# Kernel tuning notes

Measured on AMD Instinct MI355X. Metric: run time of the kernel, lower is better.

## Reference

```python
import jax, jax.numpy as jnp
import numpy as np

B, DIM, H, W = 4, 192, 256, 256
HEADS, DS = 6, 2
CPH = DIM // HEADS  # channels per head = 32
DN = ('NCHW', 'OIHW', 'NCHW')


def _conv(x, w, padding, groups=1):
    return jax.lax.conv_general_dilated(x, w, (1, 1), padding,
                                        dimension_numbers=DN,
                                        feature_group_count=groups)


def setup_inputs() -> dict:
    key = jax.random.key(0)
    ks = jax.random.split(key, 5)
    x = jax.random.normal(ks[0], (B, DIM, H, W), dtype=jnp.float32)
    temperature = jnp.ones((HEADS, 1, 1), dtype=jnp.float32)
    qkv_w = jax.random.normal(ks[1], (3 * DIM, DIM, 1, 1), dtype=jnp.float32) * 0.02
    dw_w = jax.random.normal(ks[2], (3 * DIM, 1, 3, 3), dtype=jnp.float32) * 0.02
    proj_w = jax.random.normal(ks[3], (DIM, DIM, 1, 1), dtype=jnp.float32) * 0.02
    a = jnp.full((1,), 0.2, dtype=jnp.float32)
    return {"x": x, "temperature": temperature, "qkv_w": qkv_w, "dw_w": dw_w,
            "proj_w": proj_w, "a1": a, "a2": a, "a3": a, "a4": a}


def _masked_softmax(attn, kk):
    # top-k mask per row (exact torch.topk + scatter_ semantics)
    _, idx = jax.lax.top_k(attn, kk)                      # [b,h,C,kk]
    mask = jax.nn.one_hot(idx, attn.shape[-1], dtype=jnp.bool_).any(axis=-2)
    return jax.nn.softmax(jnp.where(mask, attn, -jnp.inf), axis=-1)


def reference(x, temperature, qkv_w, dw_w, proj_w, a1, a2, a3, a4):
    b, c, h, w = x.shape
    h2, w2 = h // DS, w // DS
    # 1x1 qkv conv at full res, then exact adaptive (regular) max pool by DS
    qkv = _conv(x, qkv_w, 'VALID')                        # [b, 3*dim, h, w]
    qkv = jax.lax.reduce_window(qkv, -jnp.inf, jax.lax.max,
                                (1, 1, DS, DS), (1, 1, DS, DS), 'VALID')
    # depthwise 3x3
    qkv = _conv(qkv, dw_w, 'SAME', groups=3 * DIM)        # [b, 3*dim, h2, w2]
    q, k, v = jnp.split(qkv, 3, axis=1)
    n = h2 * w2
    q = q.reshape(b, HEADS, CPH, n)
    k = k.reshape(b, HEADS, CPH, n)
    v = v.reshape(b, HEADS, CPH, n)
    # F.normalize along last dim (eps clamp 1e-12)
    q = q / jnp.maximum(jnp.linalg.norm(q, axis=-1, keepdims=True), 1e-12)
    k = k / jnp.maximum(jnp.linalg.norm(k, axis=-1, keepdims=True), 1e-12)
    attn = jnp.einsum('bhcn,bhdn->bhcd', q, k) * temperature[None]  # [b,h,C,C]
    Cc = attn.shape[-1]
    att1 = _masked_softmax(attn, Cc // 2)
    att2 = _masked_softmax(attn, Cc * 2 // 3)
    att3 = _masked_softmax(attn, Cc * 3 // 4)
    att4 = _masked_softmax(attn, Cc * 4 // 5)
    def apply(a):
        return jnp.einsum('bhcd,bhdn->bhcn', a, v)
    out = apply(att1) * a1 + apply(att2) * a2 + apply(att3) * a3 + apply(att4) * a4
    out = out.reshape(b, DIM, h2, w2)
    out = jax.nn.gelu(out, approximate=False)
    # nearest upsample by integer factor DS
    out = jnp.repeat(jnp.repeat(out, DS, axis=2), DS, axis=3)
    out = _conv(out, proj_w, 'VALID')
    return out
```

## Files before the change

kernel.cpp:

```cpp
#include <hip/hip_runtime.h>
#include <hip/hip_bf16.h>
#include <math.h>

typedef __attribute__((ext_vector_type(8))) short bf16x8;
typedef __attribute__((ext_vector_type(4))) float f32x4;
typedef __attribute__((ext_vector_type(4))) unsigned int u32x4;

#define NP 16384
#define HWFULL 65536

__device__ __forceinline__ unsigned short f2bf(float f){
    union { float f; unsigned int u; } v; v.f = f;
    unsigned int u = v.u;
    u += 0x7fffu + ((u >> 16) & 1u);
    return (unsigned short)(u >> 16);
}
__device__ __forceinline__ float bf2f(unsigned short h){
    union { unsigned int u; float f; } v; v.u = ((unsigned int)h) << 16;
    return v.f;
}
__device__ __forceinline__ unsigned int pk2(float a, float b){
    return (unsigned int)f2bf(a) | ((unsigned int)f2bf(b) << 16);
}

__global__ void k_convert(const float* __restrict__ s, unsigned short* __restrict__ d, int n){
    int i = blockIdx.x * 256 + threadIdx.x;
    if (i < n) d[i] = f2bf(s[i]);
}

__global__ __launch_bounds__(256, 2)
void k_qkvpool(const float* __restrict__ x, const unsigned short* __restrict__ Wbf,
               unsigned short* __restrict__ qkvp){
    __shared__ unsigned short Bl[128*200];
    __shared__ unsigned short Ep[192*36];
    int tid = threadIdx.x;
    int lane = tid & 63, wv = tid >> 6;
    int n16 = lane & 15, quad = lane >> 4;
    int bx = blockIdx.x;
    int y2 = bx >> 2, x2blk = bx & 3;
    int b = blockIdx.y;

    #pragma unroll 6
    for (int j=0;j<12;j++){
        int idx = tid + j*256;
        int g = idx >> 7, w = idx & 127;
        int y = y2*2 + (w >> 6);
        int xc = x2blk*64 + (w & 63);
        const float* xp = x + (size_t)(b*192 + g*8) * HWFULL + y*256 + xc;
        float v0 = xp[0];
        float v1 = xp[(size_t)1*HWFULL];
        float v2 = xp[(size_t)2*HWFULL];
        float v3 = xp[(size_t)3*HWFULL];
        float v4 = xp[(size_t)4*HWFULL];
        float v5 = xp[(size_t)5*HWFULL];
        float v6 = xp[(size_t)6*HWFULL];
        float v7 = xp[(size_t)7*HWFULL];
        u32x4 pk;
        pk.x = pk2(v0,v1); pk.y = pk2(v2,v3); pk.z = pk2(v4,v5); pk.w = pk2(v6,v7);
        *(u32x4*)&Bl[w*200 + g*8] = pk;
    }
    bf16x8 afc[3], afn[3];
    #pragma unroll
    for (int j=0;j<3;j++)
        afc[j] = *(const bf16x8*)(Wbf + (size_t)(((wv*3+j)*16 + n16)*192 + quad*8));
    __syncthreads();

    for (int ocblk=0; ocblk<3; ocblk++){
        f32x4 acc[3][8];
        #pragma unroll
        for (int j=0;j<3;j++)
          #pragma unroll
          for (int s=0;s<8;s++)
            acc[j][s] = (f32x4){0.f,0.f,0.f,0.f};

        #pragma unroll 1
        for (int it=0; it<6; it++){
            int nocb = (it==5) ? ocblk+1 : ocblk;
            int nit  = (it==5) ? 0 : it+1;
            if (nocb < 3){
                #pragma unroll
                for (int j=0;j<3;j++)
                    afn[j] = *(const bf16x8*)(Wbf +
                        (size_t)((nocb*192 + (wv*3+j)*16 + n16)*192 + nit*32 + quad*8));
            }
            int bko = it*32 + quad*8;
            bf16x8 bfr[8];
            #pragma unroll
            for (int s=0;s<8;s++) bfr[s] = *(const bf16x8*)&Bl[(s*16 + n16)*200 + bko];
            #pragma unroll
            for (int j=0;j<3;j++)
              #pragma unroll
              for (int s=0;s<8;s++)
                acc[j][s] = __builtin_amdgcn_mfma_f32_16x16x32_bf16(afc[j], bfr[s], acc[j][s], 0,0,0);
            #pragma unroll
            for (int j=0;j<3;j++) afc[j] = afn[j];
        }
        __syncthreads();
        #pragma unroll
        for (int j=0;j<3;j++){
            int ocr = (wv*3+j)*16 + quad*4;
            #pragma unroll
            for (int sp=0;sp<4;sp++){
                #pragma unroll
                for (int r=0;r<4;r++){
                    float v = fmaxf(acc[j][sp][r], acc[j][sp+4][r]);
                    float o = __shfl_xor(v, 1, 64);
                    v = fmaxf(v, o);
                    if ((n16 & 1) == 0)
                        Ep[(ocr + r)*36 + sp*8 + (n16 >> 1)] = f2bf(v);
                }
            }
        }
        __syncthreads();
        size_t rowbase = (size_t)(b*576 + ocblk*192)*NP + y2*128 + x2blk*32;
        #pragma unroll
        for (int it=0; it<6; it++){
            int c = tid + it*256;
            int row = c >> 3, seg = c & 7;
            uint2 vv = *(const uint2*)&Ep[row*36 + seg*4];
            *(uint2*)(qkvp + rowbase + (size_t)row*NP + seg*4) = vv;
        }
    }
}

__global__ void k_dwconv(const unsigned short* __restrict__ qkvp, const float* __restrict__ dww,
                         float* __restrict__ dwout, float* __restrict__ sumsq){
    __shared__ float sl[18*130];
    int tid = threadIdx.x;
    int y0 = blockIdx.x * 16;
    int ch = blockIdx.y;
    int b  = blockIdx.z;
    const unsigned short* in = qkvp + (size_t)(b*576 + ch) * NP;
    #pragma unroll
    for (int j=0;j<10;j++){
        int idx = tid + j*256;
        if (idx < 18*130){
            int row = idx / 130;
            int col = idx % 130;
            int gy = y0 - 1 + row;
            int gx = col - 1;
            float v = 0.f;
            if (gy >= 0 && gy < 128 && gx >= 0 && gx < 128)
                v = bf2f(in[gy*128 + gx]);
            sl[idx] = v;
        }
    }
    float w0 = dww[ch*9+0], w1 = dww[ch*9+1], w2 = dww[ch*9+2];
    float w3 = dww[ch*9+3], w4 = dww[ch*9+4], w5 = dww[ch*9+5];
    float w6 = dww[ch*9+6], w7 = dww[ch*9+7], w8 = dww[ch*9+8];
    __syncthreads();
    float* outp = dwout + (size_t)(b*576 + ch) * NP;
    int col = tid & 127, half = tid >> 7;
    float ssq = 0.f;
    #pragma unroll
    for (int i=0;i<8;i++){
        int ry = half*8 + i;
        const float* r0 = &sl[ry*130 + col];
        float a = r0[0]*w0   + r0[1]*w1   + r0[2]*w2
                + r0[130]*w3 + r0[131]*w4 + r0[132]*w5
                + r0[260]*w6 + r0[261]*w7 + r0[262]*w8;
        outp[(y0+ry)*128 + col] = a;
        ssq += a*a;
    }
    if (ch < 384){
        #pragma unroll
        for (int off=32; off>0; off>>=1) ssq += __shfl_down(ssq, off, 64);
        if ((tid & 63) == 0) atomicAdd(&sumsq[b*384 + ch], ssq);
    }
}

__global__ __launch_bounds__(256) void k_attnraw(const float* __restrict__ dwout,
                                                 float* __restrict__ attn){
    __shared__ float sq[128*34];
    __shared__ float sk[128*34];
    int tid = threadIdx.x;
    int n0 = blockIdx.x * 512;
    int h = blockIdx.y, b = blockIdx.z;
    const float* qb = dwout + (size_t)(b*576 + h*32)*NP + n0;
    const float* kb = dwout + (size_t)(b*576 + 192 + h*32)*NP + n0;
    int s = tid >> 6, l = tid & 63;
    int c0 = (l & 7) * 4, d0 = (l >> 3) * 4;
    float acc[4][4];
    #pragma unroll
    for (int i=0;i<4;i++)
      #pragma unroll
      for (int j=0;j<4;j++) acc[i][j] = 0.f;

    for (int slc=0; slc<4; slc++){
        int nb = slc*128;
        __syncthreads();
        #pragma unroll 4
        for (int j=0;j<16;j++){
            int idx = tid + j*256;
            int r = idx >> 7, c = idx & 127;
            sq[c*34 + r] = qb[(size_t)r*NP + nb + c];
            sk[c*34 + r] = kb[(size_t)r*NP + nb + c];
        }
        __syncthreads();
        #pragma unroll 4
        for (int i=0;i<32;i++){
            int n = s*32 + i;
            const float* qp = &sq[n*34];
            const float* kp = &sk[n*34];
            float2 qa = *(const float2*)(qp + c0);
            float2 qc = *(const float2*)(qp + c0 + 2);
            float2 ka = *(const float2*)(kp + d0);
            float2 kc = *(const float2*)(kp + d0 + 2);
            float qv[4] = {qa.x, qa.y, qc.x, qc.y};
            float kv[4] = {ka.x, ka.y, kc.x, kc.y};
            #pragma unroll
            for (int ci=0;ci<4;ci++)
              #pragma unroll
              for (int di=0;di<4;di++)
                acc[ci][di] += qv[ci]*kv[di];
        }
    }
    __syncthreads();
    float* red = sq;
    #pragma unroll
    for (int ci=0;ci<4;ci++)
      #pragma unroll
      for (int di=0;di<4;di++)
        red[(s*32 + c0+ci)*33 + d0+di] = acc[ci][di];
    __syncthreads();
    float* ap = attn + (size_t)(b*6+h)*1024;
    #pragma unroll
    for (int j=0;j<4;j++){
        int o = tid + j*256;
        int c = o >> 5, d = o & 31;
        float v = red[(0*32 + c)*33 + d] + red[(1*32 + c)*33 + d]
                + red[(2*32 + c)*33 + d] + red[(3*32 + c)*33 + d];
        atomicAdd(ap + o, v);
    }
}

__global__ void k_mask_softmax(const float* __restrict__ attn, const float* __restrict__ sumsq,
                               const float* __restrict__ temp,
                               const float* __restrict__ A1, const float* __restrict__ A2,
                               const float* __restrict__ A3, const float* __restrict__ A4,
                               float* __restrict__ comb){
    __shared__ float Am[32][33];
    __shared__ float Em[32][33];
    __shared__ float qn[32], kn[32];
    __shared__ unsigned char Rm[32][32];
    int t = threadIdx.x;
    int bh = blockIdx.x;
    int b = bh / 6, h = bh % 6;
    if (t < 32){
        qn[t] = fmaxf(sqrtf(sumsq[b*384 + h*32 + t]), 1e-12f);
        kn[t] = fmaxf(sqrtf(sumsq[b*384 + 192 + h*32 + t]), 1e-12f);
    }
    __syncthreads();
    float tv = temp[h];
    const float* ap = attn + (size_t)bh*1024;
    #pragma unroll
    for (int j=0;j<16;j++){
        int idx = t + j*64;
        int c = idx >> 5, d = idx & 31;
        Am[c][d] = ap[idx] * tv / (qn[c]*kn[d]);
    }
    __syncthreads();
    if (t < 32){
        int c = t;
        float m = -1e30f;
        for (int d=0;d<32;d++) m = fmaxf(m, Am[c][d]);
        for (int d=0;d<32;d++) Em[c][d] = expf(Am[c][d] - m);
        for (int d=0;d<32;d++){
            float ad = Am[c][d];
            int rk = 0;
            for (int dd=0;dd<32;dd++){
                float av = Am[c][dd];
                rk += (av > ad) || (av == ad && dd < d);
            }
            Rm[c][d] = (unsigned char)rk;
        }
        float d0=0,d1=0,d2=0,d3=0;
        for (int d=0;d<32;d++){
            float e = Em[c][d]; int rk = Rm[c][d];
            if (rk < 16) d0 += e;
            if (rk < 21) d1 += e;
            if (rk < 24) d2 += e;
            if (rk < 25) d3 += e;
        }
        float f0 = A1[0]/d0, f1 = A2[0]/d1, f2 = A3[0]/d2, f3 = A4[0]/d3;
        float* cp = comb + (size_t)bh*1024 + c*32;
        for (int d=0;d<32;d++){
            int rk = Rm[c][d];
            float s = (rk<16?f0:0.f) + (rk<21?f1:0.f) + (rk<24?f2:0.f) + (rk<25?f3:0.f);
            cp[d] = Em[c][d] * s;
        }
    }
}

__global__ void k_applyv(const float* __restrict__ dwout, const float* __restrict__ comb,
                         unsigned short* __restrict__ gT){
    __shared__ float cm[3072];
    int tid = threadIdx.x;
    int b = blockIdx.y;
    int hz = blockIdx.z * 3;
    int n = blockIdx.x*256 + tid;
    #pragma unroll
    for (int j=0;j<12;j++) cm[tid + j*256] = comb[b*6144 + hz*1024 + tid + j*256];
    __syncthreads();
    const float* vb = dwout + (size_t)(b*576 + 384 + hz*32)*NP + n;
    unsigned short* gp = gT + (size_t)(b*NP + n)*192 + hz*32;
    #pragma unroll 1
    for (int h=0;h<3;h++){
        float v[32];
        #pragma unroll
        for (int d=0;d<32;d++) v[d] = vb[(size_t)(h*32+d)*NP];
        const float* chp = &cm[h*1024];
        #pragma unroll 1
        for (int cg=0;cg<4;cg++){
            float s[8];
            #pragma unroll
            for (int i=0;i<8;i++){
                const float* crow = chp + (cg*8+i)*32;
                float acc = 0.f;
                #pragma unroll
                for (int d=0;d<32;d++) acc += crow[d]*v[d];
                s[i] = 0.5f*acc*(1.f + erff(acc*0.70710678118654752f));
            }
            u32x4 pk;
            pk.x = pk2(s[0],s[1]); pk.y = pk2(s[2],s[3]);
            pk.z = pk2(s[4],s[5]); pk.w = pk2(s[6],s[7]);
            *(u32x4*)(gp + h*32 + cg*8) = pk;
        }
    }
}

__global__ __launch_bounds__(256, 2)
void k_proj(const unsigned short* __restrict__ gT, const unsigned short* __restrict__ Pbf,
            float* __restrict__ out){
    __shared__ unsigned short Bl[128*200];
    int tid = threadIdx.x;
    int lane = tid & 63, wv = tid >> 6;
    int n16 = lane & 15, quad = lane >> 4;
    int y2 = blockIdx.x, b = blockIdx.y;

    #pragma unroll 6
    for (int j=0;j<12;j++){
        int idx = tid + j*256;
        int r = idx / 24, g = idx - r*24;
        *(u32x4*)&Bl[r*200 + g*8] =
            *(const u32x4*)(gT + ((size_t)(b*NP + y2*128 + r)*192 + g*8));
    }
    bf16x8 afc[3], afn[3];
    #pragma unroll
    for (int j=0;j<3;j++)
        afc[j] = *(const bf16x8*)(Pbf + (size_t)(((wv*3+j)*16 + n16)*192 + quad*8));
    __syncthreads();

    f32x4 acc[3][8];
    #pragma unroll
    for (int j=0;j<3;j++)
      #pragma unroll
      for (int s=0;s<8;s++)
        acc[j][s] = (f32x4){0.f,0.f,0.f,0.f};

    #pragma unroll 1
    for (int it=0; it<6; it++){
        if (it < 5){
            #pragma unroll
            for (int j=0;j<3;j++)
                afn[j] = *(const bf16x8*)(Pbf +
                    (size_t)(((wv*3+j)*16 + n16)*192 + (it+1)*32 + quad*8));
        }
        int bko = it*32 + quad*8;
        bf16x8 bfr[8];
        #pragma unroll
        for (int s=0;s<8;s++) bfr[s] = *(const bf16x8*)&Bl[(s*16 + n16)*200 + bko];
        #pragma unroll
        for (int j=0;j<3;j++)
          #pragma unroll
          for (int s=0;s<8;s++)
            acc[j][s] = __builtin_amdgcn_mfma_f32_16x16x32_bf16(afc[j], bfr[s], acc[j][s], 0,0,0);
        #pragma unroll
        for (int j=0;j<3;j++) afc[j] = afn[j];
    }

    #pragma unroll
    for (int j=0;j<3;j++){
        int oc = (wv*3+j)*16 + quad*4;
        #pragma unroll
        for (int sp=0;sp<8;sp++){
            int x2 = sp*16 + n16;
            #pragma unroll
            for (int r=0;r<4;r++){
                float v = acc[j][sp][r];
                size_t o = ((size_t)(b*192 + oc + r)*256 + 2*y2)*256 + 2*x2;
                float2 val = make_float2(v, v);
                *(float2*)(out + o) = val;
                *(float2*)(out + o + 256) = val;
            }
        }
    }
}

extern "C" void kernel_launch(void* const* d_in, const int* in_sizes, int n_in,
                              void* d_out, int out_size, void* d_ws, size_t ws_size,
                              hipStream_t stream){
    const float* x     = (const float*)d_in[0];
    const float* temp  = (const float*)d_in[1];
    const float* qkvw  = (const float*)d_in[2];
    const float* dww   = (const float*)d_in[3];
    const float* projw = (const float*)d_in[4];
    const float* A1    = (const float*)d_in[5];
    const float* A2    = (const float*)d_in[6];
    const float* A3    = (const float*)d_in[7];
    const float* A4    = (const float*)d_in[8];
    float* out = (float*)d_out;
    char* ws = (char*)d_ws;

    float*          dwout = (float*)ws;
    unsigned short* qkvp  = (unsigned short*)(ws + 150994944ull);
    unsigned short* gT    = (unsigned short*)(ws + 150994944ull);
    unsigned short* Wbf   = (unsigned short*)(ws + 226492416ull);
    unsigned short* Pbf   = (unsigned short*)(ws + 226713600ull);
    float*          attn  = (float*)(ws + 226787328ull);
    float*          comb  = (float*)(ws + 226885632ull);
    float*          sumsq = (float*)(ws + 226983936ull);

    hipMemsetAsync(attn, 0, 98304, stream);
    hipMemsetAsync(sumsq, 0, 6144, stream);
    k_convert<<<dim3((110592+255)/256), dim3(256), 0, stream>>>(qkvw, Wbf, 110592);
    k_convert<<<dim3((36864+255)/256), dim3(256), 0, stream>>>(projw, Pbf, 36864);
    k_qkvpool<<<dim3(512,4), dim3(256), 0, stream>>>(x, Wbf, qkvp);
    k_dwconv<<<dim3(8,576,4), dim3(256), 0, stream>>>(qkvp, dww, dwout, sumsq);
    k_attnraw<<<dim3(32,6,4), dim3(256), 0, stream>>>(dwout, attn);
    k_mask_softmax<<<dim3(24), dim3(64), 0, stream>>>(attn, sumsq, temp, A1, A2, A3, A4, comb);
    k_applyv<<<dim3(64,4,2), dim3(256), 0, stream>>>(dwout, comb, gT);
    k_proj<<<dim3(128,4), dim3(256), 0, stream>>>(gT, Pbf, out);
}
```

Measured before the change: 643.9 us.

## Store depthwise output in bf16, parallelize masked softmax, vectorize dwconv loads

```diff
diff --git a/kernel.cpp b/kernel.cpp
--- a/kernel.cpp
+++ b/kernel.cpp
@@ -20,7 +20,9 @@
     return v.f;
 }
 __device__ __forceinline__ unsigned int pk2(float a, float b){
-    return (unsigned int)f2bf(a) | ((unsigned int)f2bf(b) << 16);
+    unsigned int r;
+    asm("v_cvt_pk_bf16_f32 %0, %1, %2" : "=v"(r) : "v"(a), "v"(b));
+    return r;
 }
 
 __global__ void k_convert(const float* __restrict__ s, unsigned short* __restrict__ d, int n){
@@ -114,8 +116,8 @@
         __syncthreads();
         size_t rowbase = (size_t)(b*576 + ocblk*192)*NP + y2*128 + x2blk*32;
         #pragma unroll
-        for (int it=0; it<6; it++){
-            int c = tid + it*256;
+        for (int it2=0; it2<6; it2++){
+            int c = tid + it2*256;
             int row = c >> 3, seg = c & 7;
             uint2 vv = *(const uint2*)&Ep[row*36 + seg*4];
             *(uint2*)(qkvp + rowbase + (size_t)row*NP + seg*4) = vv;
@@ -124,43 +126,51 @@
 }
 
 __global__ void k_dwconv(const unsigned short* __restrict__ qkvp, const float* __restrict__ dww,
-                         float* __restrict__ dwout, float* __restrict__ sumsq){
-    __shared__ float sl[18*130];
+                         unsigned short* __restrict__ dwoutB, float* __restrict__ sumsq){
+    __shared__ float sl[18*132];
     int tid = threadIdx.x;
     int y0 = blockIdx.x * 16;
     int ch = blockIdx.y;
     int b  = blockIdx.z;
     const unsigned short* in = qkvp + (size_t)(b*576 + ch) * NP;
-    #pragma unroll
-    for (int j=0;j<10;j++){
-        int idx = tid + j*256;
-        if (idx < 18*130){
-            int row = idx / 130;
-            int col = idx % 130;
+    int l = tid & 63, wr = tid >> 6;
+    #pragma unroll
+    for (int j=0;j<5;j++){
+        int row = wr + j*4;
+        if (row < 18){
             int gy = y0 - 1 + row;
-            int gx = col - 1;
-            float v = 0.f;
-            if (gy >= 0 && gy < 128 && gx >= 0 && gx < 128)
-                v = bf2f(in[gy*128 + gx]);
-            sl[idx] = v;
-        }
-    }
+            float2 v = make_float2(0.f, 0.f);
+            if (gy >= 0 && gy < 128){
+                unsigned int u = *(const unsigned int*)&in[gy*128 + l*2];
+                v.x = bf2f((unsigned short)(u & 0xffffu));
+                v.y = bf2f((unsigned short)(u >> 16));
+            }
+            *(float2*)&sl[row*132 + 2 + l*2] = v;
+        }
+    }
+    if (tid < 18) sl[tid*132 + 1] = 0.f;
+    else if (tid < 36) sl[(tid-18)*132 + 130] = 0.f;
     float w0 = dww[ch*9+0], w1 = dww[ch*9+1], w2 = dww[ch*9+2];
     float w3 = dww[ch*9+3], w4 = dww[ch*9+4], w5 = dww[ch*9+5];
     float w6 = dww[ch*9+6], w7 = dww[ch*9+7], w8 = dww[ch*9+8];
     __syncthreads();
-    float* outp = dwout + (size_t)(b*576 + ch) * NP;
+    unsigned short* outp = dwoutB + (size_t)(b*576 + ch) * NP;
     int col = tid & 127, half = tid >> 7;
     float ssq = 0.f;
+    int base = (half*8)*132 + col + 1;
+    float r0a=sl[base],     r0b=sl[base+1],   r0c=sl[base+2];
+    float r1a=sl[base+132], r1b=sl[base+133], r1c=sl[base+134];
     #pragma unroll
     for (int i=0;i<8;i++){
-        int ry = half*8 + i;
-        const float* r0 = &sl[ry*130 + col];
-        float a = r0[0]*w0   + r0[1]*w1   + r0[2]*w2
-                + r0[130]*w3 + r0[131]*w4 + r0[132]*w5
-                + r0[260]*w6 + r0[261]*w7 + r0[262]*w8;
-        outp[(y0+ry)*128 + col] = a;
+        const float* r2 = &sl[base + (i+2)*132];
+        float r2a=r2[0], r2b=r2[1], r2c=r2[2];
+        float a = r0a*w0 + r0b*w1 + r0c*w2
+                + r1a*w3 + r1b*w4 + r1c*w5
+                + r2a*w6 + r2b*w7 + r2c*w8;
+        outp[(y0 + half*8 + i)*128 + col] = f2bf(a);
         ssq += a*a;
+        r0a=r1a; r0b=r1b; r0c=r1c;
+        r1a=r2a; r1b=r2b; r1c=r2c;
     }
     if (ch < 384){
         #pragma unroll
@@ -169,15 +179,15 @@
     }
 }
 
-__global__ __launch_bounds__(256) void k_attnraw(const float* __restrict__ dwout,
+__global__ __launch_bounds__(256) void k_attnraw(const unsigned short* __restrict__ dwoutB,
                                                  float* __restrict__ attn){
     __shared__ float sq[128*34];
     __shared__ float sk[128*34];
     int tid = threadIdx.x;
     int n0 = blockIdx.x * 512;
     int h = blockIdx.y, b = blockIdx.z;
-    const float* qb = dwout + (size_t)(b*576 + h*32)*NP + n0;
-    const float* kb = dwout + (size_t)(b*576 + 192 + h*32)*NP + n0;
+    const unsigned short* qb = dwoutB + (size_t)(b*576 + h*32)*NP + n0;
+    const unsigned short* kb = dwoutB + (size_t)(b*576 + 192 + h*32)*NP + n0;
     int s = tid >> 6, l = tid & 63;
     int c0 = (l & 7) * 4, d0 = (l >> 3) * 4;
     float acc[4][4];
@@ -193,8 +203,8 @@
         for (int j=0;j<16;j++){
             int idx = tid + j*256;
             int r = idx >> 7, c = idx & 127;
-            sq[c*34 + r] = qb[(size_t)r*NP + nb + c];
-            sk[c*34 + r] = kb[(size_t)r*NP + nb + c];
+            sq[c*34 + r] = bf2f(qb[(size_t)r*NP + nb + c]);
+            sk[c*34 + r] = bf2f(kb[(size_t)r*NP + nb + c]);
         }
         __syncthreads();
         #pragma unroll 4
@@ -240,59 +250,48 @@
                                const float* __restrict__ A3, const float* __restrict__ A4,
                                float* __restrict__ comb){
     __shared__ float Am[32][33];
-    __shared__ float Em[32][33];
     __shared__ float qn[32], kn[32];
-    __shared__ unsigned char Rm[32][32];
     int t = threadIdx.x;
     int bh = blockIdx.x;
     int b = bh / 6, h = bh % 6;
-    if (t < 32){
-        qn[t] = fmaxf(sqrtf(sumsq[b*384 + h*32 + t]), 1e-12f);
-        kn[t] = fmaxf(sqrtf(sumsq[b*384 + 192 + h*32 + t]), 1e-12f);
-    }
-    __syncthreads();
+    if (t < 32) qn[t] = fmaxf(sqrtf(sumsq[b*384 + h*32 + t]), 1e-12f);
+    else if (t >= 64 && t < 96) kn[t-64] = fmaxf(sqrtf(sumsq[b*384 + 192 + h*32 + (t-64)]), 1e-12f);
+    __syncthreads();
+    int c = t >> 5, d = t & 31;
     float tv = temp[h];
-    const float* ap = attn + (size_t)bh*1024;
-    #pragma unroll
-    for (int j=0;j<16;j++){
-        int idx = t + j*64;
-        int c = idx >> 5, d = idx & 31;
-        Am[c][d] = ap[idx] * tv / (qn[c]*kn[d]);
-    }
-    __syncthreads();
-    if (t < 32){
-        int c = t;
-        float m = -1e30f;
-        for (int d=0;d<32;d++) m = fmaxf(m, Am[c][d]);
-        for (int d=0;d<32;d++) Em[c][d] = expf(Am[c][d] - m);
-        for (int d=0;d<32;d++){
-            float ad = Am[c][d];
-            int rk = 0;
-            for (int dd=0;dd<32;dd++){
-                float av = Am[c][dd];
-                rk += (av > ad) || (av == ad && dd < d);
-            }
-            Rm[c][d] = (unsigned char)rk;
-        }
-        float d0=0,d1=0,d2=0,d3=0;
-        for (int d=0;d<32;d++){
-            float e = Em[c][d]; int rk = Rm[c][d];
-            if (rk < 16) d0 += e;
-            if (rk < 21) d1 += e;
-            if (rk < 24) d2 += e;
-            if (rk < 25) d3 += e;
-        }
-        float f0 = A1[0]/d0, f1 = A2[0]/d1, f2 = A3[0]/d2, f3 = A4[0]/d3;
-        float* cp = comb + (size_t)bh*1024 + c*32;
-        for (int d=0;d<32;d++){
-            int rk = Rm[c][d];
-            float s = (rk<16?f0:0.f) + (rk<21?f1:0.f) + (rk<24?f2:0.f) + (rk<25?f3:0.f);
-            cp[d] = Em[c][d] * s;
-        }
-    }
-}
-
-__global__ void k_applyv(const float* __restrict__ dwout, const float* __restrict__ comb,
+    float am = attn[(size_t)bh*1024 + t] * tv / (qn[c]*kn[d]);
+    Am[c][d] = am;
+    float m = am;
+    #pragma unroll
+    for (int off=16; off>0; off>>=1) m = fmaxf(m, __shfl_down(m, off, 32));
+    m = __shfl(m, 0, 32);
+    float e = expf(am - m);
+    __syncthreads();
+    int rk = 0;
+    #pragma unroll 8
+    for (int dd=0; dd<32; dd++){
+        float av = Am[c][dd];
+        rk += (av > am) || (av == am && dd < d);
+    }
+    float e0 = rk < 16 ? e : 0.f;
+    float e1 = rk < 21 ? e : 0.f;
+    float e2 = rk < 24 ? e : 0.f;
+    float e3 = rk < 25 ? e : 0.f;
+    #pragma unroll
+    for (int off=16; off>0; off>>=1){
+        e0 += __shfl_down(e0, off, 32);
+        e1 += __shfl_down(e1, off, 32);
+        e2 += __shfl_down(e2, off, 32);
+        e3 += __shfl_down(e3, off, 32);
+    }
+    float d0 = __shfl(e0, 0, 32), d1 = __shfl(e1, 0, 32);
+    float d2 = __shfl(e2, 0, 32), d3 = __shfl(e3, 0, 32);
+    float s = (rk<16 ? A1[0]/d0 : 0.f) + (rk<21 ? A2[0]/d1 : 0.f)
+            + (rk<24 ? A3[0]/d2 : 0.f) + (rk<25 ? A4[0]/d3 : 0.f);
+    comb[(size_t)bh*1024 + t] = e * s;
+}
+
+__global__ void k_applyv(const unsigned short* __restrict__ dwoutB, const float* __restrict__ comb,
                          unsigned short* __restrict__ gT){
     __shared__ float cm[3072];
     int tid = threadIdx.x;
@@ -302,13 +301,13 @@
     #pragma unroll
     for (int j=0;j<12;j++) cm[tid + j*256] = comb[b*6144 + hz*1024 + tid + j*256];
     __syncthreads();
-    const float* vb = dwout + (size_t)(b*576 + 384 + hz*32)*NP + n;
+    const unsigned short* vb = dwoutB + (size_t)(b*576 + 384 + hz*32)*NP + n;
     unsigned short* gp = gT + (size_t)(b*NP + n)*192 + hz*32;
     #pragma unroll 1
     for (int h=0;h<3;h++){
         float v[32];
         #pragma unroll
-        for (int d=0;d<32;d++) v[d] = vb[(size_t)(h*32+d)*NP];
+        for (int d=0;d<32;d++) v[d] = bf2f(vb[(size_t)(h*32+d)*NP]);
         const float* chp = &cm[h*1024];
         #pragma unroll 1
         for (int cg=0;cg<4;cg++){
@@ -412,23 +411,23 @@
     float* out = (float*)d_out;
     char* ws = (char*)d_ws;
 
-    float*          dwout = (float*)ws;
-    unsigned short* qkvp  = (unsigned short*)(ws + 150994944ull);
-    unsigned short* gT    = (unsigned short*)(ws + 150994944ull);
-    unsigned short* Wbf   = (unsigned short*)(ws + 226492416ull);
-    unsigned short* Pbf   = (unsigned short*)(ws + 226713600ull);
-    float*          attn  = (float*)(ws + 226787328ull);
-    float*          comb  = (float*)(ws + 226885632ull);
-    float*          sumsq = (float*)(ws + 226983936ull);
+    unsigned short* dwoutB = (unsigned short*)ws;
+    unsigned short* qkvp   = (unsigned short*)(ws + 75497472ull);
+    unsigned short* gT     = (unsigned short*)(ws + 75497472ull);
+    unsigned short* Wbf    = (unsigned short*)(ws + 150994944ull);
+    unsigned short* Pbf    = (unsigned short*)(ws + 151216128ull);
+    float*          attn   = (float*)(ws + 151289856ull);
+    float*          comb   = (float*)(ws + 151388160ull);
+    float*          sumsq  = (float*)(ws + 151486464ull);
 
     hipMemsetAsync(attn, 0, 98304, stream);
     hipMemsetAsync(sumsq, 0, 6144, stream);
     k_convert<<<dim3((110592+255)/256), dim3(256), 0, stream>>>(qkvw, Wbf, 110592);
     k_convert<<<dim3((36864+255)/256), dim3(256), 0, stream>>>(projw, Pbf, 36864);
     k_qkvpool<<<dim3(512,4), dim3(256), 0, stream>>>(x, Wbf, qkvp);
-    k_dwconv<<<dim3(8,576,4), dim3(256), 0, stream>>>(qkvp, dww, dwout, sumsq);
-    k_attnraw<<<dim3(32,6,4), dim3(256), 0, stream>>>(dwout, attn);
-    k_mask_softmax<<<dim3(24), dim3(64), 0, stream>>>(attn, sumsq, temp, A1, A2, A3, A4, comb);
-    k_applyv<<<dim3(64,4,2), dim3(256), 0, stream>>>(dwout, comb, gT);
+    k_dwconv<<<dim3(8,576,4), dim3(256), 0, stream>>>(qkvp, dww, dwoutB, sumsq);
+    k_attnraw<<<dim3(32,6,4), dim3(256), 0, stream>>>(dwoutB, attn);
+    k_mask_softmax<<<dim3(24), dim3(1024), 0, stream>>>(attn, sumsq, temp, A1, A2, A3, A4, comb);
+    k_applyv<<<dim3(64,4,2), dim3(256), 0, stream>>>(dwoutB, comb, gT);
     k_proj<<<dim3(128,4), dim3(256), 0, stream>>>(gT, Pbf, out);
 }
```

After: 570.2 us. 11.5% less time.
